# Kernel tuning notes

Measured on AMD Instinct MI355X. Metric: run time of the kernel, lower is better.

The kernel has to match this reference:

```python
import jax, jax.numpy as jnp
import numpy as np

EPS = 1e-5

def layer_norm(x, g, b):
    mu = jnp.mean(x, axis=-1, keepdims=True)
    var = jnp.var(x, axis=-1, keepdims=True)
    return (x - mu) * jax.lax.rsqrt(var + EPS) * g + b

def setup_inputs() -> dict:
    key = jax.random.key(0)
    ks = jax.random.split(key, 16)
    N, E, D, ED = 50000, 500000, 128, 5
    def w(k, i, o):
        return jax.random.normal(k, (i, o), jnp.float32) / np.sqrt(i)
    return {
        "x": jax.random.normal(ks[0], (N, D), jnp.float32),
        "edge_attr": jax.random.normal(ks[1], (E, ED), jnp.float32),
        "pos": jax.random.normal(ks[2], (N, 3), jnp.float32),
        "node_w1": w(ks[3], D, D), "node_b1": jnp.zeros((D,), jnp.float32),
        "node_g1": jnp.ones((D,), jnp.float32), "node_be1": jnp.zeros((D,), jnp.float32),
        "node_w2": w(ks[4], D, D), "node_b2": jnp.zeros((D,), jnp.float32),
        "edge_w1": w(ks[5], 2 * D + ED, D), "edge_b1": jnp.zeros((D,), jnp.float32),
        "edge_g1": jnp.ones((D,), jnp.float32), "edge_be1": jnp.zeros((D,), jnp.float32),
        "edge_w2": w(ks[6], D, D), "edge_b2": jnp.zeros((D,), jnp.float32),
        "upd_w": w(ks[7], 2 * D, D), "upd_b": jnp.zeros((D,), jnp.float32),
        "ln_g": jnp.ones((D,), jnp.float32), "ln_b": jnp.zeros((D,), jnp.float32),
        "edge_index": jax.random.randint(ks[8], (2, E), 0, N, jnp.int64),
    }

def reference(x, edge_attr, pos, node_w1, node_b1, node_g1, node_be1, node_w2, node_b2,
              edge_w1, edge_b1, edge_g1, edge_be1, edge_w2, edge_b2,
              upd_w, upd_b, ln_g, ln_b, edge_index):
    N = x.shape[0]
    # node MLP: Linear -> LayerNorm -> ReLU -> Linear (dropout=0)
    h_nodes = jax.nn.relu(layer_norm(x @ node_w1 + node_b1, node_g1, node_be1)) @ node_w2 + node_b2
    src, dst = edge_index[0], edge_index[1]
    # edge MLP on gathered endpoint features + edge_attr  [E, 2D+edge_dim]
    ef = jnp.concatenate([x[src], x[dst], edge_attr], axis=1)
    h_edges = jax.nn.relu(layer_norm(ef @ edge_w1 + edge_b1, edge_g1, edge_be1)) @ edge_w2 + edge_b2
    # scatter-add aggregation to destination nodes
    h_agg = jax.ops.segment_sum(h_edges, dst, num_segments=N)
    h_out = jnp.concatenate([h_nodes, h_agg], axis=1) @ upd_w + upd_b
    h_out = h_out + x  # residual (in_channels == out_channels)
    return layer_norm(h_out, ln_g, ln_b)
```

## Files before the change

kernel.cpp:

```cpp
#include <hip/hip_runtime.h>
#include <stdint.h>

#define D    128
#define ED   5
#define BLK  512
#define WPB  8
#define W1S  296
#define W2S  136
#define HS   136
#define US   264
#define GRID 256

typedef __attribute__((ext_vector_type(8))) short bf16x8;
typedef __attribute__((ext_vector_type(4))) float f32x4;

__device__ __forceinline__ unsigned short f2bf(float f) {
    union { float f; uint32_t u; } c; c.f = f;
    uint32_t r = (c.u + 0x7fffu + ((c.u >> 16) & 1u)) >> 16;
    return (unsigned short)r;
}
__device__ __forceinline__ float bflo(uint32_t u) {
    union { uint32_t u; float f; } c; c.u = u << 16; return c.f;
}
__device__ __forceinline__ float bfhi(uint32_t u) {
    union { uint32_t u; float f; } c; c.u = u & 0xffff0000u; return c.f;
}
__device__ __forceinline__ bf16x8 cvt8(const float* __restrict__ p) {
    float4 a = *(const float4*)p;
    float4 b = *(const float4*)(p + 4);
    bf16x8 r;
    r[0] = (short)f2bf(a.x); r[1] = (short)f2bf(a.y);
    r[2] = (short)f2bf(a.z); r[3] = (short)f2bf(a.w);
    r[4] = (short)f2bf(b.x); r[5] = (short)f2bf(b.y);
    r[6] = (short)f2bf(b.z); r[7] = (short)f2bf(b.w);
    return r;
}
__device__ __forceinline__ bool detect64(const int* ei) {
    return (ei[1] == 0) & (ei[3] == 0) & (ei[5] == 0) &
           (ei[7] == 0) & (ei[9] == 0) & (ei[11] == 0);
}

__global__ __launch_bounds__(256)
void cvt_x_kernel(const float* __restrict__ in, unsigned short* __restrict__ out, int n8) {
    int i = blockIdx.x * blockDim.x + threadIdx.x;
    if (i >= n8) return;
    float4 a = ((const float4*)in)[2 * i];
    float4 b = ((const float4*)in)[2 * i + 1];
    union { unsigned short s[8]; uint4 v; } p;
    p.s[0] = f2bf(a.x); p.s[1] = f2bf(a.y); p.s[2] = f2bf(a.z); p.s[3] = f2bf(a.w);
    p.s[4] = f2bf(b.x); p.s[5] = f2bf(b.y); p.s[6] = f2bf(b.z); p.s[7] = f2bf(b.w);
    ((uint4*)out)[i] = p.v;
}

__global__ __launch_bounds__(512)
void count_kernel(const int* __restrict__ ei, int* __restrict__ cnt, int E) {
    const bool is64 = detect64(ei);
    int e = blockIdx.x * 512 + threadIdx.x;
    if (e >= E) return;
    int d = is64 ? ei[2 * ((size_t)E + e)] : ei[(size_t)E + e];
    atomicAdd(&cnt[d], 1);
}

__global__ __launch_bounds__(1024)
void scan_blk_kernel(const int* __restrict__ cnt, int* __restrict__ part,
                     int* __restrict__ bsum, int N) {
    __shared__ int wsum[16];
    const int tid = threadIdx.x, wave = tid >> 6, lane = tid & 63;
    const int idx = blockIdx.x * 1024 + tid;
    int v = (idx < N) ? cnt[idx] : 0;
    int s = v;
    #pragma unroll
    for (int off = 1; off < 64; off <<= 1) {
        int t = __shfl_up(s, off, 64);
        if (lane >= off) s += t;
    }
    if (lane == 63) wsum[wave] = s;
    __syncthreads();
    if (wave == 0 && lane < 16) {
        int ws_ = wsum[lane];
        #pragma unroll
        for (int off = 1; off < 16; off <<= 1) {
            int t = __shfl_up(ws_, off, 64);
            if (lane >= off) ws_ += t;
        }
        wsum[lane] = ws_;
    }
    __syncthreads();
    const int excl = ((wave == 0) ? 0 : wsum[wave - 1]) + (s - v);
    if (idx < N) part[idx] = excl;
    if (tid == 0) bsum[blockIdx.x] = wsum[15];
}

__global__ __launch_bounds__(1024)
void scan_top_kernel(int* __restrict__ bsum, int nb) {
    __shared__ int wsum[16];
    const int tid = threadIdx.x, wave = tid >> 6, lane = tid & 63;
    int v = (tid < nb) ? bsum[tid] : 0;
    int s = v;
    #pragma unroll
    for (int off = 1; off < 64; off <<= 1) {
        int t = __shfl_up(s, off, 64);
        if (lane >= off) s += t;
    }
    if (lane == 63) wsum[wave] = s;
    __syncthreads();
    if (wave == 0 && lane < 16) {
        int ws_ = wsum[lane];
        #pragma unroll
        for (int off = 1; off < 16; off <<= 1) {
            int t = __shfl_up(ws_, off, 64);
            if (lane >= off) ws_ += t;
        }
        wsum[lane] = ws_;
    }
    __syncthreads();
    const int excl = ((wave == 0) ? 0 : wsum[wave - 1]) + (s - v);
    if (tid < nb) bsum[tid] = excl;
}

__global__ __launch_bounds__(1024)
void scan_add_kernel(const int* __restrict__ part, const int* __restrict__ bsum,
                     int* __restrict__ starts, int* __restrict__ cursor,
                     int N, int E) {
    const int idx = blockIdx.x * 1024 + threadIdx.x;
    if (idx < N) {
        int v = part[idx] + bsum[blockIdx.x];
        starts[idx] = v;
        cursor[idx] = v;
    }
    if (blockIdx.x == 0 && threadIdx.x == 0) starts[N] = E;
}

__global__ __launch_bounds__(512)
void fill_kernel(const int* __restrict__ ei, int* __restrict__ cursor,
                 int* __restrict__ eids, int E) {
    const bool is64 = detect64(ei);
    int e = blockIdx.x * 512 + threadIdx.x;
    if (e >= E) return;
    int d = is64 ? ei[2 * ((size_t)E + e)] : ei[(size_t)E + e];
    int pos = atomicAdd(&cursor[d], 1);
    eids[pos] = e;
}

__global__ __launch_bounds__(512)
void agg_kernel(const unsigned short* __restrict__ h2, const int* __restrict__ starts,
                const int* __restrict__ eids, unsigned short* __restrict__ aggb, int N) {
    const int wid = blockIdx.x * WPB + (threadIdx.x >> 6);
    if (wid >= N) return;
    const int lane = threadIdx.x & 63;
    const int s = starts[wid], t = starts[wid + 1];
    float a0 = 0.f, a1 = 0.f, b0 = 0.f, b1 = 0.f;
    float p0 = 0.f, p1 = 0.f, q0 = 0.f, q1 = 0.f;
    int j = s;
    for (; j + 4 <= t; j += 4) {
        const int e0 = eids[j], e1 = eids[j + 1], e2 = eids[j + 2], e3 = eids[j + 3];
        uint32_t u0 = *(const uint32_t*)(h2 + (size_t)e0 * D + 2 * lane);
        uint32_t u1 = *(const uint32_t*)(h2 + (size_t)e1 * D + 2 * lane);
        uint32_t u2 = *(const uint32_t*)(h2 + (size_t)e2 * D + 2 * lane);
        uint32_t u3 = *(const uint32_t*)(h2 + (size_t)e3 * D + 2 * lane);
        a0 += bflo(u0); a1 += bfhi(u0);
        b0 += bflo(u1); b1 += bfhi(u1);
        p0 += bflo(u2); p1 += bfhi(u2);
        q0 += bflo(u3); q1 += bfhi(u3);
    }
    for (; j < t; ++j) {
        const int e = eids[j];
        uint32_t u = *(const uint32_t*)(h2 + (size_t)e * D + 2 * lane);
        a0 += bflo(u); a1 += bfhi(u);
    }
    const float r0 = (a0 + b0) + (p0 + q0);
    const float r1 = (a1 + b1) + (p1 + q1);
    uint32_t o = (uint32_t)f2bf(r0) | ((uint32_t)f2bf(r1) << 16);
    *(uint32_t*)(aggb + (size_t)wid * D + 2 * lane) = o;
}

template<bool EDGE, bool XBF, bool CSR>
__global__ __launch_bounds__(BLK, 2)
void mlp_kernel(const float* __restrict__ x, const unsigned short* __restrict__ xbf,
                const float* __restrict__ ea, const int* __restrict__ ei,
                const float* __restrict__ w1, const float* __restrict__ b1,
                const float* __restrict__ g1, const float* __restrict__ be1,
                const float* __restrict__ w2, const float* __restrict__ b2,
                unsigned short* __restrict__ hout, float* __restrict__ aggf,
                int N, int E)
{
    __shared__ unsigned short w1t[128 * W1S];
    __shared__ unsigned short w2t[128 * W2S];
    __shared__ unsigned short hb[WPB][16 * HS];

    const int tid = threadIdx.x;
    const int KROWS = EDGE ? 288 : 128;
    for (int i = tid; i < KROWS * 128; i += BLK) {
        int k = i >> 7, n = i & 127;
        float v = (!EDGE || k < (2 * D + ED)) ? w1[k * 128 + n] : 0.f;
        w1t[n * W1S + k] = f2bf(v);
    }
    for (int i = tid; i < 128 * 128; i += BLK) {
        int k = i >> 7, n = i & 127;
        w2t[n * W2S + k] = f2bf(w2[k * 128 + n]);
    }
    __syncthreads();

    bool is64 = false;
    if (EDGE) is64 = detect64(ei);

    const int lane = tid & 63, w = tid >> 6;
    const int g = lane >> 4, c = lane & 15;

    float b1v[8], g1v[8], e1v[8], b2v[8];
    #pragma unroll
    for (int nt = 0; nt < 8; ++nt) {
        b1v[nt] = b1[nt * 16 + c];  g1v[nt] = g1[nt * 16 + c];
        e1v[nt] = be1[nt * 16 + c]; b2v[nt] = b2[nt * 16 + c];
    }

    const int cnt = EDGE ? E : N;
    const int nT = (cnt + 15) >> 4;
    const int step = gridDim.x * WPB;
    unsigned short* hw = hb[w];

    int pdd = 0, prc = 0;
    size_t paoff = 0, pboff = 0;
    bf16x8 pf[9];

    auto loadIdx = [&](int tl) {
        const int rr = tl * 16 + c;
        const int rc = rr < cnt ? rr : cnt - 1;
        prc = rc;
        if (EDGE) {
            int s = is64 ? ei[2 * (size_t)rc]       : ei[rc];
            pdd   = is64 ? ei[2 * ((size_t)E + rc)] : ei[(size_t)E + rc];
            paoff = (size_t)s * D;
            pboff = (size_t)pdd * D;
        } else {
            paoff = (size_t)rc * D;
        }
    };
    auto loadFrags = [&]() {
        #pragma unroll
        for (int kk = 0; kk < (EDGE ? 8 : 4); ++kk) {
            const size_t o = (kk < 4) ? paoff + kk * 32 : pboff + (kk - 4) * 32;
            if (XBF) pf[kk] = *(const bf16x8*)(xbf + o + 8 * g);
            else     pf[kk] = cvt8(x + o + 8 * g);
        }
        if (EDGE) {
            bf16x8 t;
            #pragma unroll
            for (int j = 0; j < 8; ++j) t[j] = 0;
            if (g == 0) {
                #pragma unroll
                for (int j = 0; j < ED; ++j)
                    t[j] = (short)f2bf(ea[(size_t)prc * ED + j]);
            }
            pf[8] = t;
        }
    };

    int tile = blockIdx.x * WPB + w;
    if (tile < nT) { loadIdx(tile); loadFrags(); }

    for (; tile < nT; tile += step) {
        bf16x8 af[9];
        #pragma unroll
        for (int kk = 0; kk < (EDGE ? 9 : 4); ++kk) af[kk] = pf[kk];
        const int dd = pdd;
        const int row = tile * 16 + c;

        const int tn = tile + step;
        loadIdx(tn < nT ? tn : tile);

        const f32x4 z = {0.f, 0.f, 0.f, 0.f};
        f32x4 acc[8] = {z, z, z, z, z, z, z, z};
        #pragma unroll
        for (int kk = 0; kk < (EDGE ? 9 : 4); ++kk) {
            const unsigned short* wr = &w1t[c * W1S + kk * 32 + 8 * g];
            #pragma unroll
            for (int nt = 0; nt < 8; ++nt) {
                bf16x8 bf = *(const bf16x8*)(wr + nt * 16 * W1S);
                acc[nt] = __builtin_amdgcn_mfma_f32_16x16x32_bf16(af[kk], bf, acc[nt], 0, 0, 0);
            }
        }

        loadFrags();

        float mean[4], rstd[4];
        #pragma unroll
        for (int r = 0; r < 4; ++r) {
            float s = 0.f, q = 0.f;
            #pragma unroll
            for (int nt = 0; nt < 8; ++nt) {
                float v = acc[nt][r] + b1v[nt];
                acc[nt][r] = v;
                s += v; q += v * v;
            }
            s += __shfl_xor(s, 1, 64); q += __shfl_xor(q, 1, 64);
            s += __shfl_xor(s, 2, 64); q += __shfl_xor(q, 2, 64);
            s += __shfl_xor(s, 4, 64); q += __shfl_xor(q, 4, 64);
            s += __shfl_xor(s, 8, 64); q += __shfl_xor(q, 8, 64);
            float m = s * (1.f / 128.f);
            float var = q * (1.f / 128.f) - m * m;
            mean[r] = m;
            rstd[r] = rsqrtf(var + 1e-5f);
        }
        #pragma unroll
        for (int nt = 0; nt < 8; ++nt) {
            #pragma unroll
            for (int r = 0; r < 4; ++r) {
                float h = fmaxf((acc[nt][r] - mean[r]) * rstd[r] * g1v[nt] + e1v[nt], 0.f);
                hw[(4 * g + r) * HS + nt * 16 + c] = f2bf(h);
            }
        }

        f32x4 acc2[8] = {z, z, z, z, z, z, z, z};
        #pragma unroll
        for (int kk = 0; kk < 4; ++kk) {
            bf16x8 hf = *(const bf16x8*)&hw[c * HS + kk * 32 + 8 * g];
            const unsigned short* wr = &w2t[c * W2S + kk * 32 + 8 * g];
            #pragma unroll
            for (int nt = 0; nt < 8; ++nt) {
                bf16x8 bf = *(const bf16x8*)(wr + nt * 16 * W2S);
                acc2[nt] = __builtin_amdgcn_mfma_f32_16x16x32_bf16(hf, bf, acc2[nt], 0, 0, 0);
            }
        }

        if (EDGE && !CSR) {
            int dv[4];
            #pragma unroll
            for (int r = 0; r < 4; ++r) dv[r] = __shfl(dd, 4 * g + r, 64);
            #pragma unroll
            for (int r = 0; r < 4; ++r) {
                const int er = tile * 16 + 4 * g + r;
                if (er < cnt) {
                    float* dst = aggf + (size_t)dv[r] * D + c;
                    #pragma unroll
                    for (int nt = 0; nt < 8; ++nt)
                        atomicAdd(dst + nt * 16, acc2[nt][r] + b2v[nt]);
                }
            }
        } else {
            #pragma unroll
            for (int nt = 0; nt < 8; ++nt) {
                #pragma unroll
                for (int r = 0; r < 4; ++r)
                    hw[(4 * g + r) * HS + nt * 16 + c] = f2bf(acc2[nt][r] + b2v[nt]);
            }
            if (row < cnt) {
                unsigned short* dst = hout + (size_t)row * D;
                #pragma unroll
                for (int j = 0; j < 4; ++j)
                    *(uint4*)(dst + (j * 4 + g) * 8) =
                        *(const uint4*)&hw[c * HS + (j * 4 + g) * 8];
            }
        }
    }
}

template<bool AGGBF, bool XBF>
__global__ __launch_bounds__(BLK, 4)
void upd2_kernel(const unsigned short* __restrict__ hnb, const void* __restrict__ aggp,
                 const float* __restrict__ x, const unsigned short* __restrict__ xbf,
                 const float* __restrict__ uw, const float* __restrict__ ub,
                 const float* __restrict__ lg, const float* __restrict__ lb,
                 float* __restrict__ out, int N)
{
    __shared__ unsigned short wt[128 * US];
    const int tid = threadIdx.x;
    for (int i = tid; i < 256 * 128; i += BLK) {
        int k = i >> 7, n = i & 127;
        wt[n * US + k] = f2bf(uw[i]);
    }
    __syncthreads();

    const int lane = tid & 63, w = tid >> 6;
    const int g = lane >> 4, c = lane & 15;

    float ubv[8], gv[8], bv[8];
    #pragma unroll
    for (int nt = 0; nt < 8; ++nt) {
        ubv[nt] = ub[nt * 16 + c]; gv[nt] = lg[nt * 16 + c]; bv[nt] = lb[nt * 16 + c];
    }

    const int nT = (N + 15) >> 4;
    for (int tile = blockIdx.x * WPB + w; tile < nT; tile += gridDim.x * WPB) {
        const int row = tile * 16 + c;
        const int rc  = row < N ? row : N - 1;

        const f32x4 z = {0.f, 0.f, 0.f, 0.f};
        f32x4 acc[8] = {z, z, z, z, z, z, z, z};

        #pragma unroll
        for (int kk = 0; kk < 8; ++kk) {
            bf16x8 af;
            if (kk < 4) {
                af = *(const bf16x8*)(hnb + (size_t)rc * D + kk * 32 + 8 * g);
            } else {
                if (AGGBF)
                    af = *(const bf16x8*)((const unsigned short*)aggp +
                                          (size_t)rc * D + (kk - 4) * 32 + 8 * g);
                else
                    af = cvt8((const float*)aggp + (size_t)rc * D + (kk - 4) * 32 + 8 * g);
            }
            const unsigned short* wr = &wt[c * US + kk * 32 + 8 * g];
            #pragma unroll
            for (int nt = 0; nt < 8; ++nt) {
                bf16x8 bf = *(const bf16x8*)(wr + nt * 16 * US);
                acc[nt] = __builtin_amdgcn_mfma_f32_16x16x32_bf16(af, bf, acc[nt], 0, 0, 0);
            }
        }

        float mean[4], rstd[4];
        #pragma unroll
        for (int r = 0; r < 4; ++r) {
            const int row4 = tile * 16 + 4 * g + r;
            const int r4c = row4 < N ? row4 : N - 1;
            float s = 0.f, q = 0.f;
            #pragma unroll
            for (int nt = 0; nt < 8; ++nt) {
                float xr;
                if (XBF) xr = bflo((uint32_t)xbf[(size_t)r4c * D + nt * 16 + c]);
                else     xr = x[(size_t)r4c * D + nt * 16 + c];
                float v = acc[nt][r] + ubv[nt] + xr;
                acc[nt][r] = v;
                s += v; q += v * v;
            }
            s += __shfl_xor(s, 1, 64); q += __shfl_xor(q, 1, 64);
            s += __shfl_xor(s, 2, 64); q += __shfl_xor(q, 2, 64);
            s += __shfl_xor(s, 4, 64); q += __shfl_xor(q, 4, 64);
            s += __shfl_xor(s, 8, 64); q += __shfl_xor(q, 8, 64);
            float m = s * (1.f / 128.f);
            mean[r] = m;
            rstd[r] = rsqrtf(q * (1.f / 128.f) - m * m + 1e-5f);
        }
        #pragma unroll
        for (int r = 0; r < 4; ++r) {
            const int row4 = tile * 16 + 4 * g + r;
            if (row4 < N) {
                #pragma unroll
                for (int nt = 0; nt < 8; ++nt)
                    out[(size_t)row4 * D + nt * 16 + c] =
                        (acc[nt][r] - mean[r]) * rstd[r] * gv[nt] + bv[nt];
            }
        }
    }
}

extern "C" void kernel_launch(void* const* d_in, const int* in_sizes, int n_in,
                              void* d_out, int out_size, void* d_ws, size_t ws_size,
                              hipStream_t stream)
{
    const float* x    = (const float*)d_in[0];
    const float* ea   = (const float*)d_in[1];
    const float* nw1  = (const float*)d_in[3];
    const float* nb1  = (const float*)d_in[4];
    const float* ng1  = (const float*)d_in[5];
    const float* nbe1 = (const float*)d_in[6];
    const float* nw2  = (const float*)d_in[7];
    const float* nb2  = (const float*)d_in[8];
    const float* ew1  = (const float*)d_in[9];
    const float* eb1  = (const float*)d_in[10];
    const float* eg1  = (const float*)d_in[11];
    const float* ebe1 = (const float*)d_in[12];
    const float* ew2  = (const float*)d_in[13];
    const float* eb2  = (const float*)d_in[14];
    const float* uw   = (const float*)d_in[15];
    const float* ub   = (const float*)d_in[16];
    const float* lg   = (const float*)d_in[17];
    const float* lb   = (const float*)d_in[18];
    const int*   eidx = (const int*)d_in[19];

    const int N = in_sizes[0] / D;
    const int E = in_sizes[1] / ED;

    char* base = (char*)d_ws;
    size_t off = 0;
    auto alloc = [&](size_t bytes) -> char* {
        char* p = base + off;
        off = (off + bytes + 255) & ~(size_t)255;
        return p;
    };

    unsigned short* hnb  = (unsigned short*)alloc((size_t)N * D * 2);
    unsigned short* aggb = (unsigned short*)alloc((size_t)N * D * 2);
    unsigned short* xbf  = (unsigned short*)alloc((size_t)N * D * 2);
    int* cnt    = (int*)alloc((size_t)N * 4);
    int* starts = (int*)alloc(((size_t)N + 1) * 4);
    int* cursor = (int*)alloc((size_t)N * 4);
    int* bsum   = (int*)alloc(1024 * 4);
    int* eids   = (int*)alloc((size_t)E * 4);
    unsigned short* h2 = (unsigned short*)alloc((size_t)E * D * 2);
    const size_t needA = off;

    const int n8 = N * D / 8;
    const int egrid = (E + 511) / 512;
    const int nb = (N + 1023) / 1024;
    const int ugrid = (((N + 15) / 16) + WPB - 1) / WPB;

    if (ws_size >= needA && nb <= 1024) {
        hipMemsetAsync(cnt, 0, (size_t)N * 4, stream);
        cvt_x_kernel<<<(n8 + 255) / 256, 256, 0, stream>>>(x, xbf, n8);
        count_kernel<<<egrid, 512, 0, stream>>>(eidx, cnt, E);
        scan_blk_kernel<<<nb, 1024, 0, stream>>>(cnt, cursor, bsum, N);
        scan_top_kernel<<<1, 1024, 0, stream>>>(bsum, nb);
        scan_add_kernel<<<nb, 1024, 0, stream>>>(cursor, bsum, starts, cursor, N, E);
        fill_kernel<<<egrid, 512, 0, stream>>>(eidx, cursor, eids, E);
        mlp_kernel<false, true, true><<<GRID, BLK, 0, stream>>>(
            x, xbf, nullptr, nullptr, nw1, nb1, ng1, nbe1, nw2, nb2, hnb, nullptr, N, E);
        mlp_kernel<true, true, true><<<GRID, BLK, 0, stream>>>(
            x, xbf, ea, eidx, ew1, eb1, eg1, ebe1, ew2, eb2, h2, nullptr, N, E);
        agg_kernel<<<(N + WPB - 1) / WPB, 512, 0, stream>>>(h2, starts, eids, aggb, N);
        upd2_kernel<true, true><<<ugrid, BLK, 0, stream>>>(
            hnb, aggb, x, xbf, uw, ub, lg, lb, (float*)d_out, N);
        return;
    }

    off = 0;
    unsigned short* hnb2 = (unsigned short*)alloc((size_t)N * D * 2);
    float* aggf = (float*)alloc((size_t)N * D * 4);
    unsigned short* xbf2 = (unsigned short*)alloc((size_t)N * D * 2);
    const size_t needB = off;

    hipMemsetAsync(aggf, 0, (size_t)N * D * 4, stream);
    if (ws_size >= needB) {
        cvt_x_kernel<<<(n8 + 255) / 256, 256, 0, stream>>>(x, xbf2, n8);
        mlp_kernel<false, true, false><<<GRID, BLK, 0, stream>>>(
            x, xbf2, nullptr, nullptr, nw1, nb1, ng1, nbe1, nw2, nb2, hnb2, nullptr, N, E);
        mlp_kernel<true, true, false><<<GRID, BLK, 0, stream>>>(
            x, xbf2, ea, eidx, ew1, eb1, eg1, ebe1, ew2, eb2, nullptr, aggf, N, E);
        upd2_kernel<false, true><<<ugrid, BLK, 0, stream>>>(
            hnb2, aggf, x, xbf2, uw, ub, lg, lb, (float*)d_out, N);
    } else {
        mlp_kernel<false, false, false><<<GRID, BLK, 0, stream>>>(
            x, nullptr, nullptr, nullptr, nw1, nb1, ng1, nbe1, nw2, nb2, hnb2, nullptr, N, E);
        mlp_kernel<true, false, false><<<GRID, BLK, 0, stream>>>(
            x, nullptr, ea, eidx, ew1, eb1, eg1, ebe1, ew2, eb2, nullptr, aggf, N, E);
        upd2_kernel<false, false><<<ugrid, BLK, 0, stream>>>(
            hnb2, aggf, x, nullptr, uw, ub, lg, lb, (float*)d_out, N);
    }
}
```

Baseline: 477.5 us.

## Write edge outputs in CSR order and swizzle LDS staging buffer

The fill kernel now stores each edge's CSR slot instead of the inverse permutation. The edge MLP writes its output row straight to that slot, so the aggregation kernel reads contiguous rows per destination node instead of gathering through an eids indirection. Separately, the per-wave LDS hidden buffer uses an XOR swizzle on 8-element chunks to reduce bank conflicts on the transposed reads. The cost is that the edge MLP's global writes become scattered rather than sequential.

```diff
diff --git a/kernel.cpp b/kernel.cpp
--- a/kernel.cpp
+++ b/kernel.cpp
@@ -133,39 +133,38 @@
 
 __global__ __launch_bounds__(512)
 void fill_kernel(const int* __restrict__ ei, int* __restrict__ cursor,
-                 int* __restrict__ eids, int E) {
+                 int* __restrict__ slotp, int E) {
     const bool is64 = detect64(ei);
     int e = blockIdx.x * 512 + threadIdx.x;
     if (e >= E) return;
     int d = is64 ? ei[2 * ((size_t)E + e)] : ei[(size_t)E + e];
-    int pos = atomicAdd(&cursor[d], 1);
-    eids[pos] = e;
+    slotp[e] = atomicAdd(&cursor[d], 1);
 }
 
 __global__ __launch_bounds__(512)
 void agg_kernel(const unsigned short* __restrict__ h2, const int* __restrict__ starts,
-                const int* __restrict__ eids, unsigned short* __restrict__ aggb, int N) {
+                unsigned short* __restrict__ aggb, int N) {
     const int wid = blockIdx.x * WPB + (threadIdx.x >> 6);
     if (wid >= N) return;
     const int lane = threadIdx.x & 63;
     const int s = starts[wid], t = starts[wid + 1];
+    const unsigned short* p = h2 + (size_t)s * D + 2 * lane;
+    const int n = t - s;
     float a0 = 0.f, a1 = 0.f, b0 = 0.f, b1 = 0.f;
     float p0 = 0.f, p1 = 0.f, q0 = 0.f, q1 = 0.f;
-    int j = s;
-    for (; j + 4 <= t; j += 4) {
-        const int e0 = eids[j], e1 = eids[j + 1], e2 = eids[j + 2], e3 = eids[j + 3];
-        uint32_t u0 = *(const uint32_t*)(h2 + (size_t)e0 * D + 2 * lane);
-        uint32_t u1 = *(const uint32_t*)(h2 + (size_t)e1 * D + 2 * lane);
-        uint32_t u2 = *(const uint32_t*)(h2 + (size_t)e2 * D + 2 * lane);
-        uint32_t u3 = *(const uint32_t*)(h2 + (size_t)e3 * D + 2 * lane);
+    int j = 0;
+    for (; j + 4 <= n; j += 4) {
+        uint32_t u0 = *(const uint32_t*)(p + (size_t)(j + 0) * D);
+        uint32_t u1 = *(const uint32_t*)(p + (size_t)(j + 1) * D);
+        uint32_t u2 = *(const uint32_t*)(p + (size_t)(j + 2) * D);
+        uint32_t u3 = *(const uint32_t*)(p + (size_t)(j + 3) * D);
         a0 += bflo(u0); a1 += bfhi(u0);
         b0 += bflo(u1); b1 += bfhi(u1);
         p0 += bflo(u2); p1 += bfhi(u2);
         q0 += bflo(u3); q1 += bfhi(u3);
     }
-    for (; j < t; ++j) {
-        const int e = eids[j];
-        uint32_t u = *(const uint32_t*)(h2 + (size_t)e * D + 2 * lane);
+    for (; j < n; ++j) {
+        uint32_t u = *(const uint32_t*)(p + (size_t)j * D);
         a0 += bflo(u); a1 += bfhi(u);
     }
     const float r0 = (a0 + b0) + (p0 + q0);
@@ -178,6 +177,7 @@
 __global__ __launch_bounds__(BLK, 2)
 void mlp_kernel(const float* __restrict__ x, const unsigned short* __restrict__ xbf,
                 const float* __restrict__ ea, const int* __restrict__ ei,
+                const int* __restrict__ slotp,
                 const float* __restrict__ w1, const float* __restrict__ b1,
                 const float* __restrict__ g1, const float* __restrict__ be1,
                 const float* __restrict__ w2, const float* __restrict__ b2,
@@ -219,7 +219,7 @@
     const int step = gridDim.x * WPB;
     unsigned short* hw = hb[w];
 
-    int pdd = 0, prc = 0;
+    int pdd = 0, prc = 0, psl = 0;
     size_t paoff = 0, pboff = 0;
     bf16x8 pf[9];
 
@@ -232,6 +232,7 @@
             pdd   = is64 ? ei[2 * ((size_t)E + rc)] : ei[(size_t)E + rc];
             paoff = (size_t)s * D;
             pboff = (size_t)pdd * D;
+            if (CSR) psl = slotp[rc];
         } else {
             paoff = (size_t)rc * D;
         }
@@ -264,6 +265,7 @@
         #pragma unroll
         for (int kk = 0; kk < (EDGE ? 9 : 4); ++kk) af[kk] = pf[kk];
         const int dd = pdd;
+        const int sl = psl;
         const int row = tile * 16 + c;
 
         const int tn = tile + step;
@@ -307,14 +309,15 @@
             #pragma unroll
             for (int r = 0; r < 4; ++r) {
                 float h = fmaxf((acc[nt][r] - mean[r]) * rstd[r] * g1v[nt] + e1v[nt], 0.f);
-                hw[(4 * g + r) * HS + nt * 16 + c] = f2bf(h);
+                const int rw = 4 * g + r;
+                hw[rw * HS + ((nt * 2 + (c >> 3)) ^ ((rw >> 1) & 7)) * 8 + (c & 7)] = f2bf(h);
             }
         }
 
         f32x4 acc2[8] = {z, z, z, z, z, z, z, z};
         #pragma unroll
         for (int kk = 0; kk < 4; ++kk) {
-            bf16x8 hf = *(const bf16x8*)&hw[c * HS + kk * 32 + 8 * g];
+            bf16x8 hf = *(const bf16x8*)&hw[c * HS + ((4 * kk + g) ^ ((c >> 1) & 7)) * 8];
             const unsigned short* wr = &w2t[c * W2S + kk * 32 + 8 * g];
             #pragma unroll
             for (int nt = 0; nt < 8; ++nt) {
@@ -341,15 +344,19 @@
             #pragma unroll
             for (int nt = 0; nt < 8; ++nt) {
                 #pragma unroll
-                for (int r = 0; r < 4; ++r)
-                    hw[(4 * g + r) * HS + nt * 16 + c] = f2bf(acc2[nt][r] + b2v[nt]);
+                for (int r = 0; r < 4; ++r) {
+                    const int rw = 4 * g + r;
+                    hw[rw * HS + ((nt * 2 + (c >> 3)) ^ ((rw >> 1) & 7)) * 8 + (c & 7)] =
+                        f2bf(acc2[nt][r] + b2v[nt]);
+                }
             }
             if (row < cnt) {
-                unsigned short* dst = hout + (size_t)row * D;
+                const int orow = (EDGE && CSR) ? sl : row;
+                unsigned short* dst = hout + (size_t)orow * D;
                 #pragma unroll
                 for (int j = 0; j < 4; ++j)
                     *(uint4*)(dst + (j * 4 + g) * 8) =
-                        *(const uint4*)&hw[c * HS + (j * 4 + g) * 8];
+                        *(const uint4*)&hw[c * HS + ((j * 4 + g) ^ ((c >> 1) & 7)) * 8];
             }
         }
     }
@@ -486,7 +493,7 @@
     int* starts = (int*)alloc(((size_t)N + 1) * 4);
     int* cursor = (int*)alloc((size_t)N * 4);
     int* bsum   = (int*)alloc(1024 * 4);
-    int* eids   = (int*)alloc((size_t)E * 4);
+    int* slotA  = (int*)alloc((size_t)E * 4);
     unsigned short* h2 = (unsigned short*)alloc((size_t)E * D * 2);
     const size_t needA = off;
 
@@ -502,12 +509,14 @@
         scan_blk_kernel<<<nb, 1024, 0, stream>>>(cnt, cursor, bsum, N);
         scan_top_kernel<<<1, 1024, 0, stream>>>(bsum, nb);
         scan_add_kernel<<<nb, 1024, 0, stream>>>(cursor, bsum, starts, cursor, N, E);
-        fill_kernel<<<egrid, 512, 0, stream>>>(eidx, cursor, eids, E);
+        fill_kernel<<<egrid, 512, 0, stream>>>(eidx, cursor, slotA, E);
         mlp_kernel<false, true, true><<<GRID, BLK, 0, stream>>>(
-            x, xbf, nullptr, nullptr, nw1, nb1, ng1, nbe1, nw2, nb2, hnb, nullptr, N, E);
+            x, xbf, nullptr, nullptr, nullptr, nw1, nb1, ng1, nbe1, nw2, nb2,
+            hnb, nullptr, N, E);
         mlp_kernel<true, true, true><<<GRID, BLK, 0, stream>>>(
-            x, xbf, ea, eidx, ew1, eb1, eg1, ebe1, ew2, eb2, h2, nullptr, N, E);
-        agg_kernel<<<(N + WPB - 1) / WPB, 512, 0, stream>>>(h2, starts, eids, aggb, N);
+            x, xbf, ea, eidx, slotA, ew1, eb1, eg1, ebe1, ew2, eb2,
+            h2, nullptr, N, E);
+        agg_kernel<<<(N + WPB - 1) / WPB, 512, 0, stream>>>(h2, starts, aggb, N);
         upd2_kernel<true, true><<<ugrid, BLK, 0, stream>>>(
             hnb, aggb, x, xbf, uw, ub, lg, lb, (float*)d_out, N);
         return;
@@ -523,16 +532,20 @@
     if (ws_size >= needB) {
         cvt_x_kernel<<<(n8 + 255) / 256, 256, 0, stream>>>(x, xbf2, n8);
         mlp_kernel<false, true, false><<<GRID, BLK, 0, stream>>>(
-            x, xbf2, nullptr, nullptr, nw1, nb1, ng1, nbe1, nw2, nb2, hnb2, nullptr, N, E);
+            x, xbf2, nullptr, nullptr, nullptr, nw1, nb1, ng1, nbe1, nw2, nb2,
+            hnb2, nullptr, N, E);
         mlp_kernel<true, true, false><<<GRID, BLK, 0, stream>>>(
-            x, xbf2, ea, eidx, ew1, eb1, eg1, ebe1, ew2, eb2, nullptr, aggf, N, E);
+            x, xbf2, ea, eidx, nullptr, ew1, eb1, eg1, ebe1, ew2, eb2,
+            nullptr, aggf, N, E);
         upd2_kernel<false, true><<<ugrid, BLK, 0, stream>>>(
             hnb2, aggf, x, xbf2, uw, ub, lg, lb, (float*)d_out, N);
     } else {
         mlp_kernel<false, false, false><<<GRID, BLK, 0, stream>>>(
-            x, nullptr, nullptr, nullptr, nw1, nb1, ng1, nbe1, nw2, nb2, hnb2, nullptr, N, E);
+            x, nullptr, nullptr, nullptr, nullptr, nw1, nb1, ng1, nbe1, nw2, nb2,
+            hnb2, nullptr, N, E);
         mlp_kernel<true, false, false><<<GRID, BLK, 0, stream>>>(
-            x, nullptr, ea, eidx, ew1, eb1, eg1, ebe1, ew2, eb2, nullptr, aggf, N, E);
+            x, nullptr, ea, eidx, nullptr, ew1, eb1, eg1, ebe1, ew2, eb2,
+            nullptr, aggf, N, E);
         upd2_kernel<false, false><<<ugrid, BLK, 0, stream>>>(
             hnb2, aggf, x, nullptr, uw, ub, lg, lb, (float*)d_out, N);
     }
```

Measured after the change: 469.6 us. Within noise of the previous version (-1.7%).
